# Kernel tuning notes

Hardware: AMD Instinct MI355X
Metric: run time of the kernel (lower is better)

Reference implementation:

```python
import jax, jax.numpy as jnp
import numpy as np

B, C, S, H, W = 64, 768, 8, 28, 28

def setup_inputs() -> dict:
    key = jax.random.key(0)
    k1, k2, k3 = jax.random.split(key, 3)
    x = jax.random.normal(k1, (B, C, H, W), dtype=jnp.float32)
    # Conv2d(token_dim -> num_region, k=3, pad=1); torch default init scale ~ 1/sqrt(fan_in)
    fan_in = C * 3 * 3
    bound = 1.0 / np.sqrt(fan_in)
    conv_w = jax.random.uniform(k2, (S, C, 3, 3), dtype=jnp.float32, minval=-bound, maxval=bound)
    conv_b = jax.random.uniform(k3, (S,), dtype=jnp.float32, minval=-bound, maxval=bound)
    return {"x": x, "conv_w": conv_w, "conv_b": conv_b}

def reference(x, conv_w, conv_b):
    # spatial attention conv: [B,C,H,W] -> [B,S,H,W]
    region_mask = jax.lax.conv_general_dilated(
        x, conv_w, window_strides=(1, 1), padding=((1, 1), (1, 1)),
        dimension_numbers=("NCHW", "OIHW", "NCHW"))
    region_mask = region_mask + conv_b[None, :, None, None]
    # fused per-region weighted global average pooling:
    # for each region s: mean over HW of x * mask_s  ==> single batched contraction
    hw = x.shape[2] * x.shape[3]
    learned_regions = jnp.einsum("bchw,bshw->bcs", x, region_mask) / hw  # [B,C,S]
    return learned_regions, region_mask
```

## Files before the change

kernel.cpp:

```cpp
#include <hip/hip_runtime.h>

#define B_ 64
#define C_ 768
#define S_ 8
#define HW_ 784
#define CPB_ 48
#define NCHUNK_ 16
#define CSTEP_ 4
#define NSTEP_ 12
#define ROWS_ 16
#define FW_ 30
#define FRH_ (ROWS_ * FW_)

__global__ __launch_bounds__(256) void wtrans_k(
    const float* __restrict__ w, float* __restrict__ wT)
{
  int idx = blockIdx.x * 256 + threadIdx.x;
  int c = idx / 72, r = idx - c * 72;
  int s = r / 9,  t = r - s * 9;
  wT[idx] = w[(size_t)s * (C_ * 9) + c * 9 + t];
}

__global__ __launch_bounds__(256) void conv_k(
    const float* __restrict__ x, const float* __restrict__ wT,
    float* __restrict__ mask_acc)
{
  __shared__ float xb[CSTEP_ * FRH_];
  const int tid = threadIdx.x;
  const int b   = blockIdx.x;
  const int c0  = blockIdx.y * CPB_;
  const int h0  = blockIdx.z * 14;
  const bool act = tid < 196;
  const int duo = act ? tid : 0;
  const int hl  = duo / 14;
  const int w2  = (duo - hl * 14) * 2;
  const int pb  = (hl + 1) * FW_ + (w2 + 1);

  for (int i = tid; i < CSTEP_ * FRH_; i += 256) xb[i] = 0.0f;

  const float4* src4 = (const float4*)(x + ((size_t)b * C_ + c0) * HW_);

  float acc[2][S_];
  #pragma unroll
  for (int px = 0; px < 2; ++px)
    #pragma unroll
    for (int s = 0; s < S_; ++s) acc[px][s] = 0.0f;

  for (int k = 0; k < NSTEP_; ++k) {
    __syncthreads();
    #pragma unroll
    for (int r = 0; r < 2; ++r) {
      int i4 = tid + r * 256;
      if (i4 < CSTEP_ * ROWS_ * 7) {
        int cl = i4 / 112, rr = i4 - cl * 112;
        int fr = rr / 7, c4 = rr - fr * 7;
        int gr = h0 - 1 + fr;
        if (gr >= 0 && gr < 28) {
          float4 v = src4[(k * CSTEP_ + cl) * 196 + gr * 7 + c4];
          float* d = &xb[cl * FRH_ + fr * FW_ + c4 * 4 + 1];
          d[0] = v.x; d[1] = v.y; d[2] = v.z; d[3] = v.w;
        }
      }
    }
    __syncthreads();

    if (act) {
      #pragma unroll
      for (int cl = 0; cl < CSTEP_; ++cl) {
        const float* f = &xb[cl * FRH_ + pb];
        float xv[3][4];
        #pragma unroll
        for (int r3 = 0; r3 < 3; ++r3)
          #pragma unroll
          for (int m = 0; m < 4; ++m)
            xv[r3][m] = f[(r3 - 1) * FW_ - 1 + m];

        const float4* wrow = (const float4*)(wT + (size_t)(c0 + k * CSTEP_ + cl) * 72);
        float wa[36];
        #pragma unroll
        for (int i = 0; i < 9; ++i) ((float4*)wa)[i] = wrow[i];
        #pragma unroll
        for (int s = 0; s < 4; ++s)
          #pragma unroll
          for (int px = 0; px < 2; ++px) {
            float a = acc[px][s];
            #pragma unroll
            for (int r3 = 0; r3 < 3; ++r3)
              #pragma unroll
              for (int kx = 0; kx < 3; ++kx)
                a = fmaf(xv[r3][px + kx], wa[s * 9 + r3 * 3 + kx], a);
            acc[px][s] = a;
          }
        #pragma unroll
        for (int i = 0; i < 9; ++i) ((float4*)wa)[i] = wrow[9 + i];
        #pragma unroll
        for (int s = 0; s < 4; ++s)
          #pragma unroll
          for (int px = 0; px < 2; ++px) {
            float a = acc[px][s + 4];
            #pragma unroll
            for (int r3 = 0; r3 < 3; ++r3)
              #pragma unroll
              for (int kx = 0; kx < 3; ++kx)
                a = fmaf(xv[r3][px + kx], wa[s * 9 + r3 * 3 + kx], a);
            acc[px][s + 4] = a;
          }
      }
    }
  }

  if (act) {
    float* dst = mask_acc + (size_t)b * S_ * HW_ + (h0 + hl) * 28 + w2;
    #pragma unroll
    for (int s = 0; s < S_; ++s)
      #pragma unroll
      for (int px = 0; px < 2; ++px)
        atomicAdd(dst + (size_t)s * HW_ + px, acc[px][s]);
  }
}

__global__ __launch_bounds__(256) void mask_bias_k(
    const float* __restrict__ mask_acc, const float* __restrict__ bias,
    float* __restrict__ outM)
{
  int i4 = blockIdx.x * 256 + threadIdx.x;
  float4 v = ((const float4*)mask_acc)[i4];
  int s = (i4 / 196) & 7;
  float bv = bias[s];
  v.x += bv; v.y += bv; v.z += bv; v.w += bv;
  ((float4*)outM)[i4] = v;
}

__global__ __launch_bounds__(256) void einsum_k(
    const float* __restrict__ x, const float* __restrict__ mask_acc,
    const float* __restrict__ bias, float* __restrict__ out)
{
  __shared__ float xs[64 * 128];
  __shared__ float ms[8 * 112];
  const int tid = threadIdx.x;
  const int cx  = blockIdx.x;
  const int b   = blockIdx.y;
  const int c0  = cx * 64;
  const int q   = tid >> 6;
  const int cl  = tid & 63;

  float acc[S_];
  #pragma unroll
  for (int s = 0; s < S_; ++s) acc[s] = 0.0f;
  float sumx = 0.0f;

  const float4* src4 = (const float4*)(x + ((size_t)b * C_ + c0) * HW_);
  const float*  mrow = mask_acc + (size_t)b * S_ * HW_;

  for (int rnd = 0; rnd < 7; ++rnd) {
    __syncthreads();
    #pragma unroll
    for (int r = 0; r < 7; ++r) {
      int i4 = tid + r * 256;
      int c = i4 / 28, jf = i4 - c * 28;
      float4 v = src4[c * 196 + rnd * 28 + jf];
      *(float4*)&xs[c * 128 + (jf ^ (c & 15)) * 4] = v;
    }
    if (tid < 224) {
      int s = tid / 28, jf = tid - s * 28;
      float4 v = *(const float4*)(mrow + (size_t)s * HW_ + rnd * 112 + jf * 4);
      *(float4*)&ms[s * 112 + jf * 4] = v;
    }
    __syncthreads();

    #pragma unroll
    for (int t = 0; t < 7; ++t) {
      const int jf = q + t * 4;
      float4 xa = *(const float4*)&xs[cl * 128 + (jf ^ (cl & 15)) * 4];
      sumx += xa.x + xa.y + xa.z + xa.w;
      #pragma unroll
      for (int s = 0; s < S_; ++s) {
        float4 m = *(const float4*)&ms[s * 112 + jf * 4];
        float a = acc[s];
        a = fmaf(xa.x, m.x, a); a = fmaf(xa.y, m.y, a);
        a = fmaf(xa.z, m.z, a); a = fmaf(xa.w, m.w, a);
        acc[s] = a;
      }
    }
  }

  __syncthreads();
  float* red = xs;
  #pragma unroll
  for (int s = 0; s < S_; ++s) red[tid * 9 + s] = acc[s];
  red[tid * 9 + 8] = sumx;
  __syncthreads();

  for (int i = tid; i < 64 * S_; i += 256) {
    int c = i >> 3, s = i & 7;
    float vs = 0.0f, vx = 0.0f;
    #pragma unroll
    for (int qq = 0; qq < 4; ++qq) {
      vs += red[(qq * 64 + c) * 9 + s];
      vx += red[(qq * 64 + c) * 9 + 8];
    }
    out[((size_t)b * C_ + c0 + c) * S_ + s] = (vs + bias[s] * vx) * (1.0f / HW_);
  }
}

extern "C" void kernel_launch(void* const* d_in, const int* in_sizes, int n_in,
                              void* d_out, int out_size, void* d_ws, size_t ws_size,
                              hipStream_t stream) {
  const float* x    = (const float*)d_in[0];
  const float* w    = (const float*)d_in[1];
  const float* bias = (const float*)d_in[2];
  float* out  = (float*)d_out;
  float* outM = out + (size_t)B_ * C_ * S_;
  float* acc  = (float*)d_ws;
  float* wT   = acc + (size_t)B_ * S_ * HW_;

  hipMemsetAsync(acc, 0, (size_t)B_ * S_ * HW_ * sizeof(float), stream);
  wtrans_k<<<(C_ * 72) / 256, 256, 0, stream>>>(w, wT);
  conv_k<<<dim3(B_, NCHUNK_, 2), 256, 0, stream>>>(x, wT, acc);
  mask_bias_k<<<(B_ * S_ * HW_ / 4 + 255) / 256, 256, 0, stream>>>(acc, bias, outM);
  einsum_k<<<dim3(12, B_), 256, 0, stream>>>(x, acc, bias, out);
}
```

Before: 344.4 us.

## Rewrite conv to direct global loads with LDS weights and einsum to per-wave shuffle reduction

The conv kernel no longer stages x tiles in shared memory. Each thread now loads its 4x3 neighbourhood straight from global memory (relying on cache) with clamped offsets and masks, while the block's 48-channel weight slice, transposed to tap-major/region-minor order, sits in LDS. The einsum kernel drops the shared-memory tiling and instead gives each wavefront two channels, reading the mask from global memory and reducing with wavefront shuffles. The aim is fewer syncs and less LDS traffic, at the cost of more redundant global/L2 reads and lower data reuse.

```diff
diff --git a/kernel.cpp b/kernel.cpp
--- a/kernel.cpp
+++ b/kernel.cpp
@@ -6,39 +6,64 @@
 #define HW_ 784
 #define CPB_ 48
 #define NCHUNK_ 16
-#define CSTEP_ 4
-#define NSTEP_ 12
-#define ROWS_ 16
-#define FW_ 30
-#define FRH_ (ROWS_ * FW_)
 
 __global__ __launch_bounds__(256) void wtrans_k(
-    const float* __restrict__ w, float* __restrict__ wT)
+    const float* __restrict__ w, float* __restrict__ wT2)
 {
   int idx = blockIdx.x * 256 + threadIdx.x;
   int c = idx / 72, r = idx - c * 72;
-  int s = r / 9,  t = r - s * 9;
-  wT[idx] = w[(size_t)s * (C_ * 9) + c * 9 + t];
+  int t = r / 8, s = r - t * 8;
+  wT2[idx] = w[(size_t)s * (C_ * 9) + c * 9 + t];
 }
 
 __global__ __launch_bounds__(256) void conv_k(
-    const float* __restrict__ x, const float* __restrict__ wT,
+    const float* __restrict__ x, const float* __restrict__ wT2,
     float* __restrict__ mask_acc)
 {
-  __shared__ float xb[CSTEP_ * FRH_];
+  __shared__ float wl[CPB_ * 72];
   const int tid = threadIdx.x;
-  const int b   = blockIdx.x;
   const int c0  = blockIdx.y * CPB_;
-  const int h0  = blockIdx.z * 14;
-  const bool act = tid < 196;
-  const int duo = act ? tid : 0;
-  const int hl  = duo / 14;
-  const int w2  = (duo - hl * 14) * 2;
-  const int pb  = (hl + 1) * FW_ + (w2 + 1);
-
-  for (int i = tid; i < CSTEP_ * FRH_; i += 256) xb[i] = 0.0f;
-
-  const float4* src4 = (const float4*)(x + ((size_t)b * C_ + c0) * HW_);
+
+  {
+    const float4* wsrc = (const float4*)(wT2 + (size_t)c0 * 72);
+    float4* wd = (float4*)wl;
+    #pragma unroll
+    for (int r = 0; r < 4; ++r) {
+      int i = tid + r * 256;
+      if (i < CPB_ * 18) wd[i] = wsrc[i];
+    }
+  }
+  __syncthreads();
+
+  const int flat = blockIdx.x * 256 + tid;
+  const int b    = flat / 392;
+  const int pr   = flat - b * 392;
+  const int h2   = pr / 28;
+  const int wI   = pr - h2 * 28;
+  const int h    = h2 * 2;
+
+  int ro[4]; float rm[4];
+  #pragma unroll
+  for (int dr = 0; dr < 4; ++dr) {
+    int r = h - 1 + dr;
+    rm[dr] = (r >= 0 && r < 28) ? 1.0f : 0.0f;
+    ro[dr] = min(max(r, 0), 27) * 28;
+  }
+  int co[3]; float cm[3];
+  #pragma unroll
+  for (int dc = 0; dc < 3; ++dc) {
+    int cc = wI - 1 + dc;
+    cm[dc] = (cc >= 0 && cc < 28) ? 1.0f : 0.0f;
+    co[dc] = min(max(cc, 0), 27);
+  }
+  int   eoff[12]; float msk[12];
+  #pragma unroll
+  for (int dr = 0; dr < 4; ++dr)
+    #pragma unroll
+    for (int dc = 0; dc < 3; ++dc) {
+      eoff[dr * 3 + dc] = ro[dr] + co[dc];
+      msk[dr * 3 + dc]  = rm[dr] * cm[dc];
+    }
 
   float acc[2][S_];
   #pragma unroll
@@ -46,77 +71,49 @@
     #pragma unroll
     for (int s = 0; s < S_; ++s) acc[px][s] = 0.0f;
 
-  for (int k = 0; k < NSTEP_; ++k) {
-    __syncthreads();
-    #pragma unroll
-    for (int r = 0; r < 2; ++r) {
-      int i4 = tid + r * 256;
-      if (i4 < CSTEP_ * ROWS_ * 7) {
-        int cl = i4 / 112, rr = i4 - cl * 112;
-        int fr = rr / 7, c4 = rr - fr * 7;
-        int gr = h0 - 1 + fr;
-        if (gr >= 0 && gr < 28) {
-          float4 v = src4[(k * CSTEP_ + cl) * 196 + gr * 7 + c4];
-          float* d = &xb[cl * FRH_ + fr * FW_ + c4 * 4 + 1];
-          d[0] = v.x; d[1] = v.y; d[2] = v.z; d[3] = v.w;
-        }
+  int xoff = (b * C_ + c0) * HW_;
+
+  for (int cl = 0; cl < CPB_; ++cl, xoff += HW_) {
+    float xv[12];
+    #pragma unroll
+    for (int t = 0; t < 12; ++t)
+      xv[t] = x[xoff + eoff[t]] * msk[t];
+
+    const float4* wrow = (const float4*)&wl[cl * 72];
+    #pragma unroll
+    for (int ky = 0; ky < 3; ++ky)
+      #pragma unroll
+      for (int kx = 0; kx < 3; ++kx) {
+        const int t9 = ky * 3 + kx;
+        float4 wa = wrow[t9 * 2];
+        float4 wb = wrow[t9 * 2 + 1];
+        float x0 = xv[ky * 3 + kx];
+        float x1 = xv[(ky + 1) * 3 + kx];
+        acc[0][0] = fmaf(x0, wa.x, acc[0][0]);
+        acc[0][1] = fmaf(x0, wa.y, acc[0][1]);
+        acc[0][2] = fmaf(x0, wa.z, acc[0][2]);
+        acc[0][3] = fmaf(x0, wa.w, acc[0][3]);
+        acc[0][4] = fmaf(x0, wb.x, acc[0][4]);
+        acc[0][5] = fmaf(x0, wb.y, acc[0][5]);
+        acc[0][6] = fmaf(x0, wb.z, acc[0][6]);
+        acc[0][7] = fmaf(x0, wb.w, acc[0][7]);
+        acc[1][0] = fmaf(x1, wa.x, acc[1][0]);
+        acc[1][1] = fmaf(x1, wa.y, acc[1][1]);
+        acc[1][2] = fmaf(x1, wa.z, acc[1][2]);
+        acc[1][3] = fmaf(x1, wa.w, acc[1][3]);
+        acc[1][4] = fmaf(x1, wb.x, acc[1][4]);
+        acc[1][5] = fmaf(x1, wb.y, acc[1][5]);
+        acc[1][6] = fmaf(x1, wb.z, acc[1][6]);
+        acc[1][7] = fmaf(x1, wb.w, acc[1][7]);
       }
-    }
-    __syncthreads();
-
-    if (act) {
-      #pragma unroll
-      for (int cl = 0; cl < CSTEP_; ++cl) {
-        const float* f = &xb[cl * FRH_ + pb];
-        float xv[3][4];
-        #pragma unroll
-        for (int r3 = 0; r3 < 3; ++r3)
-          #pragma unroll
-          for (int m = 0; m < 4; ++m)
-            xv[r3][m] = f[(r3 - 1) * FW_ - 1 + m];
-
-        const float4* wrow = (const float4*)(wT + (size_t)(c0 + k * CSTEP_ + cl) * 72);
-        float wa[36];
-        #pragma unroll
-        for (int i = 0; i < 9; ++i) ((float4*)wa)[i] = wrow[i];
-        #pragma unroll
-        for (int s = 0; s < 4; ++s)
-          #pragma unroll
-          for (int px = 0; px < 2; ++px) {
-            float a = acc[px][s];
-            #pragma unroll
-            for (int r3 = 0; r3 < 3; ++r3)
-              #pragma unroll
-              for (int kx = 0; kx < 3; ++kx)
-                a = fmaf(xv[r3][px + kx], wa[s * 9 + r3 * 3 + kx], a);
-            acc[px][s] = a;
-          }
-        #pragma unroll
-        for (int i = 0; i < 9; ++i) ((float4*)wa)[i] = wrow[9 + i];
-        #pragma unroll
-        for (int s = 0; s < 4; ++s)
-          #pragma unroll
-          for (int px = 0; px < 2; ++px) {
-            float a = acc[px][s + 4];
-            #pragma unroll
-            for (int r3 = 0; r3 < 3; ++r3)
-              #pragma unroll
-              for (int kx = 0; kx < 3; ++kx)
-                a = fmaf(xv[r3][px + kx], wa[s * 9 + r3 * 3 + kx], a);
-            acc[px][s + 4] = a;
-          }
-      }
-    }
-  }
-
-  if (act) {
-    float* dst = mask_acc + (size_t)b * S_ * HW_ + (h0 + hl) * 28 + w2;
-    #pragma unroll
-    for (int s = 0; s < S_; ++s)
-      #pragma unroll
-      for (int px = 0; px < 2; ++px)
-        atomicAdd(dst + (size_t)s * HW_ + px, acc[px][s]);
-  }
+  }
+
+  float* dst = mask_acc + (size_t)b * S_ * HW_ + h * 28 + wI;
+  #pragma unroll
+  for (int s = 0; s < S_; ++s)
+    #pragma unroll
+    for (int px = 0; px < 2; ++px)
+      atomicAdd(dst + (size_t)s * HW_ + px * 28, acc[px][s]);
 }
 
 __global__ __launch_bounds__(256) void mask_bias_k(
@@ -135,71 +132,67 @@
     const float* __restrict__ x, const float* __restrict__ mask_acc,
     const float* __restrict__ bias, float* __restrict__ out)
 {
-  __shared__ float xs[64 * 128];
-  __shared__ float ms[8 * 112];
-  const int tid = threadIdx.x;
-  const int cx  = blockIdx.x;
-  const int b   = blockIdx.y;
-  const int c0  = cx * 64;
-  const int q   = tid >> 6;
-  const int cl  = tid & 63;
-
-  float acc[S_];
-  #pragma unroll
-  for (int s = 0; s < S_; ++s) acc[s] = 0.0f;
-  float sumx = 0.0f;
-
-  const float4* src4 = (const float4*)(x + ((size_t)b * C_ + c0) * HW_);
-  const float*  mrow = mask_acc + (size_t)b * S_ * HW_;
-
-  for (int rnd = 0; rnd < 7; ++rnd) {
-    __syncthreads();
-    #pragma unroll
-    for (int r = 0; r < 7; ++r) {
-      int i4 = tid + r * 256;
-      int c = i4 / 28, jf = i4 - c * 28;
-      float4 v = src4[c * 196 + rnd * 28 + jf];
-      *(float4*)&xs[c * 128 + (jf ^ (c & 15)) * 4] = v;
-    }
-    if (tid < 224) {
-      int s = tid / 28, jf = tid - s * 28;
-      float4 v = *(const float4*)(mrow + (size_t)s * HW_ + rnd * 112 + jf * 4);
-      *(float4*)&ms[s * 112 + jf * 4] = v;
-    }
-    __syncthreads();
-
-    #pragma unroll
-    for (int t = 0; t < 7; ++t) {
-      const int jf = q + t * 4;
-      float4 xa = *(const float4*)&xs[cl * 128 + (jf ^ (cl & 15)) * 4];
-      sumx += xa.x + xa.y + xa.z + xa.w;
-      #pragma unroll
-      for (int s = 0; s < S_; ++s) {
-        float4 m = *(const float4*)&ms[s * 112 + jf * 4];
-        float a = acc[s];
-        a = fmaf(xa.x, m.x, a); a = fmaf(xa.y, m.y, a);
-        a = fmaf(xa.z, m.z, a); a = fmaf(xa.w, m.w, a);
-        acc[s] = a;
-      }
-    }
-  }
-
-  __syncthreads();
-  float* red = xs;
-  #pragma unroll
-  for (int s = 0; s < S_; ++s) red[tid * 9 + s] = acc[s];
-  red[tid * 9 + 8] = sumx;
-  __syncthreads();
-
-  for (int i = tid; i < 64 * S_; i += 256) {
-    int c = i >> 3, s = i & 7;
-    float vs = 0.0f, vx = 0.0f;
-    #pragma unroll
-    for (int qq = 0; qq < 4; ++qq) {
-      vs += red[(qq * 64 + c) * 9 + s];
-      vx += red[(qq * 64 + c) * 9 + 8];
-    }
-    out[((size_t)b * C_ + c0 + c) * S_ + s] = (vs + bias[s] * vx) * (1.0f / HW_);
+  const int tid  = threadIdx.x;
+  const int lane = tid & 63;
+  const int wv   = tid >> 6;
+  const int b    = blockIdx.y;
+  const int c    = (blockIdx.x * 4 + wv) * 2;
+
+  const float4* xr0 = (const float4*)(x + ((size_t)b * C_ + c) * HW_);
+  const float4* xr1 = xr0 + 196;
+  const float4* mr  = (const float4*)(mask_acc + (size_t)b * S_ * HW_);
+
+  float a0[S_], a1[S_];
+  #pragma unroll
+  for (int s = 0; s < S_; ++s) { a0[s] = 0.0f; a1[s] = 0.0f; }
+  float sx0 = 0.0f, sx1 = 0.0f;
+
+  #pragma unroll
+  for (int jf = 0; jf < 3; ++jf) {
+    int j4 = jf * 64 + lane;
+    float4 xa = xr0[j4];
+    float4 xb = xr1[j4];
+    sx0 += xa.x + xa.y + xa.z + xa.w;
+    sx1 += xb.x + xb.y + xb.z + xb.w;
+    #pragma unroll
+    for (int s = 0; s < S_; ++s) {
+      float4 m = mr[s * 196 + j4];
+      a0[s] = fmaf(xa.x, m.x, fmaf(xa.y, m.y, fmaf(xa.z, m.z, fmaf(xa.w, m.w, a0[s]))));
+      a1[s] = fmaf(xb.x, m.x, fmaf(xb.y, m.y, fmaf(xb.z, m.z, fmaf(xb.w, m.w, a1[s]))));
+    }
+  }
+  if (lane < 4) {
+    int j4 = 192 + lane;
+    float4 xa = xr0[j4];
+    float4 xb = xr1[j4];
+    sx0 += xa.x + xa.y + xa.z + xa.w;
+    sx1 += xb.x + xb.y + xb.z + xb.w;
+    #pragma unroll
+    for (int s = 0; s < S_; ++s) {
+      float4 m = mr[s * 196 + j4];
+      a0[s] = fmaf(xa.x, m.x, fmaf(xa.y, m.y, fmaf(xa.z, m.z, fmaf(xa.w, m.w, a0[s]))));
+      a1[s] = fmaf(xb.x, m.x, fmaf(xb.y, m.y, fmaf(xb.z, m.z, fmaf(xb.w, m.w, a1[s]))));
+    }
+  }
+
+  #pragma unroll
+  for (int d = 1; d < 64; d <<= 1) {
+    #pragma unroll
+    for (int s = 0; s < S_; ++s) {
+      a0[s] += __shfl_xor(a0[s], d, 64);
+      a1[s] += __shfl_xor(a1[s], d, 64);
+    }
+    sx0 += __shfl_xor(sx0, d, 64);
+    sx1 += __shfl_xor(sx1, d, 64);
+  }
+
+  if (lane == 0) {
+    float* o = out + ((size_t)b * C_ + c) * S_;
+    #pragma unroll
+    for (int s = 0; s < S_; ++s) {
+      o[s]      = (a0[s] + bias[s] * sx0) * (1.0f / HW_);
+      o[S_ + s] = (a1[s] + bias[s] * sx1) * (1.0f / HW_);
+    }
   }
 }
 
@@ -212,11 +205,11 @@
   float* out  = (float*)d_out;
   float* outM = out + (size_t)B_ * C_ * S_;
   float* acc  = (float*)d_ws;
-  float* wT   = acc + (size_t)B_ * S_ * HW_;
+  float* wT2  = acc + (size_t)B_ * S_ * HW_;
 
   hipMemsetAsync(acc, 0, (size_t)B_ * S_ * HW_ * sizeof(float), stream);
-  wtrans_k<<<(C_ * 72) / 256, 256, 0, stream>>>(w, wT);
-  conv_k<<<dim3(B_, NCHUNK_, 2), 256, 0, stream>>>(x, wT, acc);
+  wtrans_k<<<(C_ * 72) / 256, 256, 0, stream>>>(w, wT2);
+  conv_k<<<dim3(98, NCHUNK_), 256, 0, stream>>>(x, wT2, acc);
   mask_bias_k<<<(B_ * S_ * HW_ / 4 + 255) / 256, 256, 0, stream>>>(acc, bias, outM);
-  einsum_k<<<dim3(12, B_), 256, 0, stream>>>(x, acc, bias, out);
-}
+  einsum_k<<<dim3(96, B_), 256, 0, stream>>>(x, acc, bias, out);
+}
```

Result: faster. 334.6 us (-2.9%).
